# Kernel tuning notes

Hardware: AMD Instinct MI355X
Metric: run time of the kernel (lower is better)

## Reference

```python
import jax, jax.numpy as jnp
import numpy as np

EMBED, IN_DIM, HID, LAYERS, NVIEW = 1024, 256, 256, 3, 6


def _lstm_layer(x_seq, Wih, Whh, bih, bhh):
    # x_seq: [BM, N, D]; torch LSTM gate order i,f,g,o
    BM = x_seq.shape[0]
    h0 = jnp.zeros((BM, HID), x_seq.dtype)
    c0 = jnp.zeros((BM, HID), x_seq.dtype)

    def step(carry, x_t):
        h, c = carry
        gates = x_t @ Wih.T + bih + h @ Whh.T + bhh  # [BM, 4H]
        i, f, g, o = jnp.split(gates, 4, axis=-1)
        c = jax.nn.sigmoid(f) * c + jax.nn.sigmoid(i) * jnp.tanh(g)
        h = jax.nn.sigmoid(o) * jnp.tanh(c)
        return (h, c), h

    _, ys = jax.lax.scan(step, (h0, c0), jnp.swapaxes(x_seq, 0, 1))
    return jnp.swapaxes(ys, 0, 1)  # [BM, N, H]


def setup_inputs() -> dict:
    key = jax.random.key(0)
    ks = jax.random.split(key, 16)
    B, M = 32, 256
    s = lambda fan: 1.0 / np.sqrt(fan)
    inp = {
        "b_x_swin": jax.random.normal(ks[0], (B, M, NVIEW, EMBED), jnp.float32),
        "b_x_conv": jax.random.normal(ks[1], (B, M, NVIEW, EMBED), jnp.float32),
        "Wc": jax.random.uniform(ks[2], (EMBED, EMBED), jnp.float32, -s(EMBED), s(EMBED)),
        "bc": jax.random.uniform(ks[3], (EMBED,), jnp.float32, -s(EMBED), s(EMBED)),
        "Win": jax.random.uniform(ks[4], (IN_DIM, EMBED), jnp.float32, -s(EMBED), s(EMBED)),
        "b_in": jax.random.uniform(ks[5], (IN_DIM,), jnp.float32, -s(EMBED), s(EMBED)),
        "Wih": jax.random.uniform(ks[6], (LAYERS, 4 * HID, IN_DIM), jnp.float32, -s(HID), s(HID)),
        "Whh": jax.random.uniform(ks[7], (LAYERS, 4 * HID, HID), jnp.float32, -s(HID), s(HID)),
        "bih": jax.random.uniform(ks[8], (LAYERS, 4 * HID), jnp.float32, -s(HID), s(HID)),
        "bhh": jax.random.uniform(ks[9], (LAYERS, 4 * HID), jnp.float32, -s(HID), s(HID)),
        "Wv": jax.random.uniform(ks[10], (1, HID), jnp.float32, -s(HID), s(HID)),
        "bv": jax.random.uniform(ks[11], (1,), jnp.float32, -s(HID), s(HID)),
        "Ws": jax.random.uniform(ks[12], (1, NVIEW), jnp.float32, -s(NVIEW), s(NVIEW)),
        "bs": jax.random.uniform(ks[13], (1,), jnp.float32, -s(NVIEW), s(NVIEW)),
    }
    return inp


def reference(b_x_swin, b_x_conv, Wc, bc, Win, b_in, Wih, Whh, bih, bhh, Wv, bv, Ws, bs):
    B, M, N, C = b_x_swin.shape
    # fc_conv + exact GELU + residual (vectorized over all samples; same math as per-sample loop)
    x = b_x_swin + jax.nn.gelu(b_x_conv @ Wc.T + bc, approximate=False)
    x = x @ Win.T + b_in                         # [B, M, N, IN_DIM]
    x = x.reshape(B * M, N, IN_DIM)              # LSTM batch = B*M, seq = N
    for l in range(LAYERS):
        x = _lstm_layer(x, Wih[l], Whh[l], bih[l], bhh[l])
    v = (x @ Wv.T + bv).reshape(B, M, N)         # fc_viewport + flatten(1)
    score = (v @ Ws.T + bs).squeeze(-1)          # fc_score -> [B, M]
    return jnp.mean(score, axis=1)               # torch.mean per sample -> [B]
```

## Files before the change

### kernel.cpp

```cpp
#include <hip/hip_runtime.h>
#include <math.h>
#include <stdint.h>

typedef unsigned short u16;
typedef float f32x4 __attribute__((ext_vector_type(4)));
typedef short bf16x8 __attribute__((ext_vector_type(8)));

#define NVIEW 6

__device__ __forceinline__ u16 f2bf(float f){
  unsigned u = __float_as_uint(f);
  u += 0x7FFFu + ((u >> 16) & 1u);
  return (u16)(u >> 16);
}
__device__ __forceinline__ float bf2f(u16 h){
  return __uint_as_float(((unsigned)h) << 16);
}
__device__ __forceinline__ float fsig(float x){
  x = fminf(fmaxf(x, -30.f), 30.f);
  return 1.0f / (1.0f + __expf(-x));
}
__device__ __forceinline__ float ftanh(float x){
  x = fminf(fmaxf(x, -15.f), 15.f);
  float e = __expf(2.0f * x);
  return (e - 1.0f) / (e + 1.0f);
}
__device__ __forceinline__ float gelu_exact(float v){
  float x  = v * 0.70710678118654752f;
  float ax = fabsf(x);
  float t  = 1.0f / fmaf(0.3275911f, ax, 1.0f);
  float p  = t * fmaf(t, fmaf(t, fmaf(t, fmaf(t, 1.061405429f, -1.453152027f),
                                      1.421413741f), -0.284496736f), 0.254829592f);
  float er = copysignf(1.0f - p * __expf(-ax * ax), x);
  return 0.5f * v * (1.0f + er);
}
__device__ __forceinline__ void gload16(const u16* g, u16* l){
  __builtin_amdgcn_global_load_lds((const __attribute__((address_space(1))) unsigned int*)g,
                                   (__attribute__((address_space(3))) unsigned int*)l,
                                   16, 0, 0);
}

#define DSRI(dst, addr, imm) \
  asm volatile("ds_read_b128 %0, %1 offset:%2" : "=v"(dst) : "v"(addr), "i"(imm))

__global__ void k_cvt(const float* __restrict__ in, u16* __restrict__ out, long n4){
  long i = (long)blockIdx.x * blockDim.x + threadIdx.x;
  long stride = (long)gridDim.x * blockDim.x;
  for (; i < n4; i += stride){
    const float4 v = ((const float4*)in)[i];
    ushort4 o;
    o.x = f2bf(v.x); o.y = f2bf(v.y); o.z = f2bf(v.z); o.w = f2bf(v.w);
    ((ushort4*)out)[i] = o;
  }
}

__global__ void k_build_wl(const float* __restrict__ Wih, const float* __restrict__ Whh,
                           u16* __restrict__ Wl){
  int idx = blockIdx.x * 256 + threadIdx.x;
  int l   = idx >> 19;
  int rem = idx & 524287;
  int ro  = rem >> 9;
  int k   = rem & 511;
  int u = ro >> 2, q = ro & 3;
  int ri = q * 256 + u;
  float v = (k < 256) ? Wih[(l * 1024 + ri) * 256 + k]
                      : Whh[(l * 1024 + ri) * 256 + (k - 256)];
  Wl[idx] = f2bf(v);
}

__global__ void k_build_bias(const float* __restrict__ bih, const float* __restrict__ bhh,
                             float* __restrict__ biasL){
  int idx = blockIdx.x * 256 + threadIdx.x;
  if (idx < 3072){
    int l = idx >> 10; int ro = idx & 1023;
    int u = ro >> 2, q = ro & 3;
    int ri = q * 256 + u;
    biasL[idx] = bih[l * 1024 + ri] + bhh[l * 1024 + ri];
  }
}

template<int EPI>
__global__ __launch_bounds__(256, 2)
void gemm_dr(const u16* __restrict__ A0, long sA0,
             const u16* __restrict__ Bm, long sB,
             int N, int K, int NBn,
             const float* __restrict__ bias,
             const float* __restrict__ resid,
             u16* __restrict__ outb)
{
  __shared__ __align__(16) u16 lA[5 * 4096];
  __shared__ __align__(16) u16 lB[5 * 4096];

  const int tid  = threadIdx.x;
  const int lane = tid & 63;
  const int wid  = tid >> 6;
  const int wm = wid >> 1, wn = wid & 1;
  const int l15 = lane & 15, lk = lane >> 4;

  const int nwg = gridDim.x;
  const int qx  = nwg >> 3;
  const int bb  = blockIdx.x;
  const int swz = (bb & 7) * qx + (bb >> 3);
  const long m0 = (long)(swz / NBn) * 128;
  const int  n0 = (swz % NBn) * 128;
  const int  NT = K >> 5;

  const int rA0 = tid >> 2;
  const int cA  = tid & 3;
  const int slog = (((rA0 & 1) << 2) | cA) ^ ((rA0 >> 1) & 7);
  const int srow = (rA0 & ~1) | (slog >> 2);
  const int scol = (slog & 3) << 3;
  const int ldst = rA0 * 32 + cA * 8;

  auto STAGE = [&](int slot, int t){
    const int kb = t << 5;
    const int so = slot * 4096;
    #pragma unroll
    for (int c = 0; c < 2; ++c){
      const int r  = c * 64 + srow;
      gload16(A0 + (m0 + r) * sA0 + (kb + scol), &lA[so + c * 2048 + ldst]);
    }
    #pragma unroll
    for (int c = 0; c < 2; ++c){
      const int r  = c * 64 + srow;
      gload16(Bm + (long)(n0 + r) * sB + (kb + scol), &lB[so + c * 2048 + ldst]);
    }
  };

  f32x4 acc[4][4];
  #pragma unroll
  for (int i = 0; i < 4; ++i)
    #pragma unroll
    for (int j = 0; j < 4; ++j)
      acc[i][j] = (f32x4){0.f, 0.f, 0.f, 0.f};

  const int spA = (((l15 & 1) << 2) | lk) ^ (l15 >> 1);
  const int rdA = (wm * 32 + (l15 >> 1)) * 64 + spA * 8;
  const int rdB = (wn * 32 + (l15 >> 1)) * 64 + spA * 8;

  auto COMPUTE = [&](int slot){
    const int so = slot * 4096;
    bf16x8 af[4], bq[4];
    #pragma unroll
    for (int mf = 0; mf < 4; ++mf)
      af[mf] = *(const bf16x8*)&lA[so + rdA + mf * 512];
    #pragma unroll
    for (int nf = 0; nf < 4; ++nf)
      bq[nf] = *(const bf16x8*)&lB[so + rdB + nf * 512];
    #pragma unroll
    for (int mf = 0; mf < 4; ++mf)
      #pragma unroll
      for (int nf = 0; nf < 4; ++nf)
        acc[mf][nf] = __builtin_amdgcn_mfma_f32_16x16x32_bf16(af[mf], bq[nf], acc[mf][nf], 0, 0, 0);
  };

  STAGE(0, 0); STAGE(1, 1); STAGE(2, 2); STAGE(3, 3);

  int sr = 0, sw = 4;
  for (int t = 0; t + 4 <= NT; ++t){
    asm volatile("s_waitcnt vmcnt(12)" ::: "memory");
    asm volatile("s_barrier" ::: "memory");
    if (t + 4 < NT){ STAGE(sw, t + 4); }
    COMPUTE(sr);
    sr = (sr == 4) ? 0 : sr + 1;
    sw = (sw == 4) ? 0 : sw + 1;
  }
  asm volatile("s_waitcnt vmcnt(8)" ::: "memory");
  asm volatile("s_barrier" ::: "memory");
  COMPUTE(sr); sr = (sr == 4) ? 0 : sr + 1;
  asm volatile("s_waitcnt vmcnt(4)" ::: "memory");
  asm volatile("s_barrier" ::: "memory");
  COMPUTE(sr); sr = (sr == 4) ? 0 : sr + 1;
  asm volatile("s_waitcnt vmcnt(0)" ::: "memory");
  asm volatile("s_barrier" ::: "memory");
  COMPUTE(sr);

  #pragma unroll
  for (int mf = 0; mf < 4; ++mf){
    #pragma unroll
    for (int nf = 0; nf < 4; ++nf){
      int  n    = n0 + wn * 64 + nf * 16 + l15;
      long mrow = m0 + wm * 64 + mf * 16 + lk * 4;
      float bz = bias[n];
      #pragma unroll
      for (int r = 0; r < 4; ++r){
        float v = acc[mf][nf][r] + bz;
        long off = (mrow + r) * N + n;
        if (EPI == 0) v = gelu_exact(v) + resid[off];
        outb[off] = f2bf(v);
      }
    }
  }
}

__global__ __launch_bounds__(512, 2)
void k_lstm(const u16* __restrict__ X0, const u16* __restrict__ Wl,
            const float* __restrict__ biasL,
            u16* __restrict__ HA, u16* __restrict__ HB)
{
  __shared__ __align__(16) u16 lA[16384];
  __shared__ __align__(16) u16 lB[3 * 16384];

  const int tid  = threadIdx.x;
  const int lane = tid & 63;
  const int wv   = tid >> 6;
  const int wr   = wv >> 2;
  const int wc   = wv & 3;
  const int l15  = lane & 15, lk = lane >> 4;
  const int axk  = l15 & 7;
  const int spB  = (((l15 & 1) << 2) | lk) ^ (l15 >> 1);
  const int a    = lane & 3;
  const int qb   = lane & ~3;
  const long R   = (long)blockIdx.x * 32;
  const int rotk = (blockIdx.x >> 3) & 15;

  const int rB = tid >> 2;
  const int cB = tid & 3;
  const int slogB = (((rB & 1) << 2) | cB) ^ ((rB >> 1) & 7);
  const int srowB = (rB & ~1) | (slogB >> 2);
  const int scolB = (slogB & 3) << 3;
  const int ldstB = rB * 32 + cB * 8;

  auto STB = [&](int P, int l){
    const int hfp  = P & 1;
    const int ktcp = ((P >> 1) + rotk) & 15;
    const int slot = P % 3;
    const u16* src = Wl + (long)l * 524288 + (long)hfp * 262144 + ktcp * 32;
    u16* dst = &lB[slot * 16384];
    #pragma unroll
    for (int ch = 0; ch < 4; ++ch)
      gload16(src + (long)(ch * 128 + srowB) * 512 + scolB, dst + ch * 4096 + ldstB);
  };

  const int xr_ = tid >> 4;
  const int xcb = tid & 15;
  const int xk  = xr_ & 7;

  const unsigned ldsA = (unsigned)(uintptr_t)&lA[0];
  const unsigned ldsB = (unsigned)(uintptr_t)&lB[0];
  const unsigned aRd  = ldsA + (unsigned)((wr * 16 + l15) * 1024);
  const unsigned bRd  = ldsB + (unsigned)((wc * 64 + (l15 >> 1)) * 128 + spB * 16);

  f32x4 acc[2][8];
  float cc[2][8];
  float bv[2][8];

  for (int l = 0; l < 3; ++l){
    const u16* xsrc = (l == 0) ? X0 : ((l == 1) ? HA : HB);
    u16* hdst = (l == 1) ? HB : HA;
    #pragma unroll
    for (int hf = 0; hf < 2; ++hf)
      #pragma unroll
      for (int nt = 0; nt < 8; ++nt){
        bv[hf][nt] = biasL[l * 1024 + hf * 512 + wc * 128 + nt * 16 + l15];
        cc[hf][nt] = 0.f;
      }
    __syncthreads();
    {
      bf16x8 z = (bf16x8){0,0,0,0,0,0,0,0};
      #pragma unroll
      for (int j = 0; j < 2; ++j){
        const int s = xcb * 2 + j;
        *(bf16x8*)&lA[xr_ * 512 + (32 + (s ^ xk)) * 8] = z;
      }
    }
    for (int t = 0; t < 6; ++t){
      bf16x8 xv[2];
      const u16* xp = xsrc + ((R + xr_) * 6 + t) * 256 + xcb * 16;
      xv[0] = *(const bf16x8*)(xp);
      xv[1] = *(const bf16x8*)(xp + 8);
      asm volatile("s_waitcnt vmcnt(0)" ::: "memory");
      #pragma unroll
      for (int hf = 0; hf < 2; ++hf)
        #pragma unroll
        for (int nt = 0; nt < 8; ++nt)
          acc[hf][nt] = (f32x4){0.f, 0.f, 0.f, 0.f};
      #pragma unroll
      for (int j = 0; j < 2; ++j){
        const int s = xcb * 2 + j;
        *(bf16x8*)&lA[xr_ * 512 + (s ^ xk) * 8] = xv[j];
      }
      STB(0, l); STB(1, l);
      asm volatile("s_waitcnt lgkmcnt(0)" ::: "memory");
      __builtin_amdgcn_s_barrier();

      for (int j = 0; j < 16; ++j){
        const int ktc = (j + rotk) & 15;
        const unsigned aAddr = aRd + (unsigned)((((ktc * 4 + lk) ^ axk)) << 4);
        #pragma unroll
        for (int hh = 0; hh < 2; ++hh){
          const int P = 2 * j + hh;
          if (P == 31) { asm volatile("s_waitcnt vmcnt(0)" ::: "memory"); }
          else         { asm volatile("s_waitcnt vmcnt(4)" ::: "memory"); }
          __builtin_amdgcn_s_barrier();
          if (P + 2 < 32) STB(P + 2, l);
          bf16x8 af, bq[8];
          DSRI(af, aAddr, 0);
          const unsigned bAddr = bRd + (unsigned)((P % 3) * 32768);
          DSRI(bq[0], bAddr, 0);
          DSRI(bq[1], bAddr, 1024);
          DSRI(bq[2], bAddr, 2048);
          DSRI(bq[3], bAddr, 3072);
          DSRI(bq[4], bAddr, 4096);
          DSRI(bq[5], bAddr, 5120);
          DSRI(bq[6], bAddr, 6144);
          DSRI(bq[7], bAddr, 7168);
          asm volatile("s_waitcnt lgkmcnt(0)" ::: "memory");
          __builtin_amdgcn_sched_barrier(0);
          __builtin_amdgcn_s_setprio(1);
          #pragma unroll
          for (int nt = 0; nt < 8; ++nt)
            acc[hh][nt] = __builtin_amdgcn_mfma_f32_16x16x32_bf16(af, bq[nt], acc[hh][nt], 0, 0, 0);
          __builtin_amdgcn_s_setprio(0);
        }
      }
      __builtin_amdgcn_s_barrier();

      #pragma unroll
      for (int hf = 0; hf < 2; ++hf)
        #pragma unroll
        for (int nt = 0; nt < 8; ++nt){
          const float bz = bv[hf][nt];
          float v0 = acc[hf][nt][0] + bz;
          float v1 = acc[hf][nt][1] + bz;
          float v2 = acc[hf][nt][2] + bz;
          float v3 = acc[hf][nt][3] + bz;
          float s0 = (a == 0) ? v0 : (a == 1) ? v1 : (a == 2) ? v2 : v3;
          float s1 = (a == 0) ? v1 : (a == 1) ? v2 : (a == 2) ? v3 : v0;
          float s2 = (a == 0) ? v2 : (a == 1) ? v3 : (a == 2) ? v0 : v1;
          float s3 = (a == 0) ? v3 : (a == 1) ? v0 : (a == 2) ? v1 : v2;
          float r0 = s0;
          float r1 = __shfl(s1, qb + ((a + 3) & 3));
          float r2 = __shfl(s2, qb + ((a + 2) & 3));
          float r3 = __shfl(s3, qb + ((a + 1) & 3));
          float wi = (a == 0) ? r0 : (a == 1) ? r1 : (a == 2) ? r2 : r3;
          float wf = (a == 1) ? r0 : (a == 2) ? r1 : (a == 3) ? r2 : r3;
          float wg = (a == 2) ? r0 : (a == 3) ? r1 : (a == 0) ? r2 : r3;
          float wo = (a == 3) ? r0 : (a == 0) ? r1 : (a == 1) ? r2 : r3;
          const int rloc = wr * 16 + lk * 4 + a;
          const int u    = hf * 128 + wc * 32 + nt * 4 + (l15 >> 2);
          float co = cc[hf][nt];
          float ii = fsig(wi), ff = fsig(wf), gg = ftanh(wg), oo = fsig(wo);
          float cn = ff * co + ii * gg;
          float hn = oo * ftanh(cn);
          cc[hf][nt] = cn;
          lA[rloc * 512 + (32 + ((u >> 3) ^ (rloc & 7))) * 8 + (u & 7)] = f2bf(hn);
        }
      asm volatile("s_waitcnt lgkmcnt(0)" ::: "memory");
      __builtin_amdgcn_s_barrier();
      #pragma unroll
      for (int j2 = 0; j2 < 2; ++j2){
        const int s = xcb * 2 + j2;
        bf16x8 hv = *(const bf16x8*)&lA[xr_ * 512 + (32 + (s ^ xk)) * 8];
        *(bf16x8*)(hdst + ((R + xr_) * 6 + t) * 256 + xcb * 16 + j2 * 8) = hv;
      }
    }
  }
}

__global__ void k_score(const u16* __restrict__ X3, const float* __restrict__ Wv,
                        const float* __restrict__ bv, const float* __restrict__ Ws,
                        const float* __restrict__ bs, float* __restrict__ score){
  int lane = threadIdx.x & 63;
  int bm = blockIdx.x * 4 + (threadIdx.x >> 6);
  const u16* row = X3 + (long)bm * (NVIEW * 256);
  float4 wv = *(const float4*)(Wv + lane * 4);
  float p = 0.f;
  #pragma unroll
  for (int n = 0; n < NVIEW; ++n){
    ushort4 xv = *(const ushort4*)(row + n * 256 + lane * 4);
    float d = bf2f(xv.x) * wv.x + bf2f(xv.y) * wv.y + bf2f(xv.z) * wv.z + bf2f(xv.w) * wv.w;
    p += Ws[n] * d;
  }
  #pragma unroll
  for (int off = 32; off; off >>= 1) p += __shfl_xor(p, off);
  if (lane == 0){
    float sw = Ws[0] + Ws[1] + Ws[2] + Ws[3] + Ws[4] + Ws[5];
    score[bm] = p + bv[0] * sw + bs[0];
  }
}

__global__ void k_mean(const float* __restrict__ score, float* __restrict__ out){
  __shared__ float red[256];
  int b = blockIdx.x, tid = threadIdx.x;
  red[tid] = score[b * 256 + tid];
  __syncthreads();
  for (int s = 128; s > 0; s >>= 1){
    if (tid < s) red[tid] += red[tid + s];
    __syncthreads();
  }
  if (tid == 0) out[b] = red[0] * (1.0f / 256.0f);
}

extern "C" void kernel_launch(void* const* d_in, const int* in_sizes, int n_in,
                              void* d_out, int out_size, void* d_ws, size_t ws_size,
                              hipStream_t stream){
  const float* swin = (const float*)d_in[0];
  const float* conv = (const float*)d_in[1];
  const float* Wc   = (const float*)d_in[2];
  const float* bc   = (const float*)d_in[3];
  const float* Win  = (const float*)d_in[4];
  const float* b_in = (const float*)d_in[5];
  const float* Wih  = (const float*)d_in[6];
  const float* Whh  = (const float*)d_in[7];
  const float* bih  = (const float*)d_in[8];
  const float* bhh  = (const float*)d_in[9];
  const float* Wv   = (const float*)d_in[10];
  const float* bv   = (const float*)d_in[11];
  const float* Ws   = (const float*)d_in[12];
  const float* bs   = (const float*)d_in[13];
  float* out = (float*)d_out;

  char* w = (char*)d_ws;
  u16*  convb = (u16*)(w);
  u16*  X0    = (u16*)(w);
  u16*  XA    = (u16*)(w + 25165824);
  u16*  XB    = (u16*)(w + 50331648);
  u16*  Y     = (u16*)(w + 100663296);
  u16*  Wcb   = (u16*)(w + 201326592);
  u16*  Winb  = (u16*)(w + 203423744);
  u16*  Wl    = (u16*)(w + 203948032);
  float* biasL= (float*)(w + 207093760);
  float* scoreb = (float*)(w + 207106560);

  k_cvt<<<4096, 256, 0, stream>>>(conv, convb, 49152L * 1024 / 4);
  k_cvt<<<512, 256, 0, stream>>>(Wc, Wcb, 1048576 / 4);
  k_cvt<<<128, 256, 0, stream>>>(Win, Winb, 262144 / 4);
  k_build_wl<<<6144, 256, 0, stream>>>(Wih, Whh, Wl);
  k_build_bias<<<12, 256, 0, stream>>>(bih, bhh, biasL);

  gemm_dr<0><<<3072, 256, 0, stream>>>(
      convb, 1024L, Wcb, 1024L, 1024, 1024, 8, bc, swin, Y);

  gemm_dr<1><<<768, 256, 0, stream>>>(
      Y, 1024L, Winb, 1024L, 256, 1024, 2, b_in, (const float*)nullptr, X0);

  k_lstm<<<256, 512, 0, stream>>>(X0, Wl, biasL, XA, XB);

  k_score<<<2048, 256, 0, stream>>>(XA, Wv, bv, Ws, bs, scoreb);
  k_mean<<<32, 256, 0, stream>>>(scoreb, out);
}
```

Measured before the change: 739.7 us.

## Load LSTM weight fragments directly from global into registers, dropping LDS staging

The LSTM recurrence kernel no longer stages gate weights into a triple-buffered shared-memory ring with global_load_lds. Each wave now loads its own weight fragments straight from global memory into a double-buffered register set. Waves are re-partitioned so that each one covers all 32 rows and 128 gate columns, instead of a 2x4 grid of 16-row slices. This removes most per-k-step barriers and the LDS round trip for weights. In exchange it raises register pressure (two 8-fragment buffers plus a larger accumulator tile) under launch_bounds(512,2), which risks spills, and it leaves global-load latency covered by only one prefetch stage.

After: 932.3 us. 1.26x slower.

```diff
diff --git a/kernel.cpp b/kernel.cpp
--- a/kernel.cpp
+++ b/kernel.cpp
@@ -39,9 +39,6 @@
                                    (__attribute__((address_space(3))) unsigned int*)l,
                                    16, 0, 0);
 }
-
-#define DSRI(dst, addr, imm) \
-  asm volatile("ds_read_b128 %0, %1 offset:%2" : "=v"(dst) : "v"(addr), "i"(imm))
 
 __global__ void k_cvt(const float* __restrict__ in, u16* __restrict__ out, long n4){
   long i = (long)blockIdx.x * blockDim.x + threadIdx.x;
@@ -199,62 +196,35 @@
             u16* __restrict__ HA, u16* __restrict__ HB)
 {
   __shared__ __align__(16) u16 lA[16384];
-  __shared__ __align__(16) u16 lB[3 * 16384];
 
   const int tid  = threadIdx.x;
   const int lane = tid & 63;
   const int wv   = tid >> 6;
-  const int wr   = wv >> 2;
-  const int wc   = wv & 3;
   const int l15  = lane & 15, lk = lane >> 4;
   const int axk  = l15 & 7;
-  const int spB  = (((l15 & 1) << 2) | lk) ^ (l15 >> 1);
   const int a    = lane & 3;
   const int qb   = lane & ~3;
   const long R   = (long)blockIdx.x * 32;
   const int rotk = (blockIdx.x >> 3) & 15;
-
-  const int rB = tid >> 2;
-  const int cB = tid & 3;
-  const int slogB = (((rB & 1) << 2) | cB) ^ ((rB >> 1) & 7);
-  const int srowB = (rB & ~1) | (slogB >> 2);
-  const int scolB = (slogB & 3) << 3;
-  const int ldstB = rB * 32 + cB * 8;
-
-  auto STB = [&](int P, int l){
-    const int hfp  = P & 1;
-    const int ktcp = ((P >> 1) + rotk) & 15;
-    const int slot = P % 3;
-    const u16* src = Wl + (long)l * 524288 + (long)hfp * 262144 + ktcp * 32;
-    u16* dst = &lB[slot * 16384];
-    #pragma unroll
-    for (int ch = 0; ch < 4; ++ch)
-      gload16(src + (long)(ch * 128 + srowB) * 512 + scolB, dst + ch * 4096 + ldstB);
-  };
+  const int gb   = wv * 128;
 
   const int xr_ = tid >> 4;
   const int xcb = tid & 15;
   const int xk  = xr_ & 7;
 
-  const unsigned ldsA = (unsigned)(uintptr_t)&lA[0];
-  const unsigned ldsB = (unsigned)(uintptr_t)&lB[0];
-  const unsigned aRd  = ldsA + (unsigned)((wr * 16 + l15) * 1024);
-  const unsigned bRd  = ldsB + (unsigned)((wc * 64 + (l15 >> 1)) * 128 + spB * 16);
-
   f32x4 acc[2][8];
   float cc[2][8];
-  float bv[2][8];
+  float bv[8];
 
   for (int l = 0; l < 3; ++l){
     const u16* xsrc = (l == 0) ? X0 : ((l == 1) ? HA : HB);
     u16* hdst = (l == 1) ? HB : HA;
-    #pragma unroll
-    for (int hf = 0; hf < 2; ++hf)
-      #pragma unroll
-      for (int nt = 0; nt < 8; ++nt){
-        bv[hf][nt] = biasL[l * 1024 + hf * 512 + wc * 128 + nt * 16 + l15];
-        cc[hf][nt] = 0.f;
-      }
+    const u16* wbase = Wl + (long)l * 524288 + (long)(gb + l15) * 512 + lk * 8;
+    #pragma unroll
+    for (int nt = 0; nt < 8; ++nt){
+      bv[nt] = biasL[l * 1024 + gb + nt * 16 + l15];
+      cc[0][nt] = 0.f; cc[1][nt] = 0.f;
+    }
     __syncthreads();
     {
       bf16x8 z = (bf16x8){0,0,0,0,0,0,0,0};
@@ -265,66 +235,72 @@
       }
     }
     for (int t = 0; t < 6; ++t){
-      bf16x8 xv[2];
+      bf16x8 xv0, xv1;
       const u16* xp = xsrc + ((R + xr_) * 6 + t) * 256 + xcb * 16;
-      xv[0] = *(const bf16x8*)(xp);
-      xv[1] = *(const bf16x8*)(xp + 8);
-      asm volatile("s_waitcnt vmcnt(0)" ::: "memory");
+      xv0 = *(const bf16x8*)(xp);
+      xv1 = *(const bf16x8*)(xp + 8);
       #pragma unroll
-      for (int hf = 0; hf < 2; ++hf)
+      for (int mt = 0; mt < 2; ++mt)
         #pragma unroll
         for (int nt = 0; nt < 8; ++nt)
-          acc[hf][nt] = (f32x4){0.f, 0.f, 0.f, 0.f};
-      #pragma unroll
-      for (int j = 0; j < 2; ++j){
-        const int s = xcb * 2 + j;
-        *(bf16x8*)&lA[xr_ * 512 + (s ^ xk) * 8] = xv[j];
+          acc[mt][nt] = (f32x4){0.f, 0.f, 0.f, 0.f};
+      {
+        const int s0 = xcb * 2;
+        *(bf16x8*)&lA[xr_ * 512 + (s0 ^ xk) * 8] = xv0;
+        *(bf16x8*)&lA[xr_ * 512 + ((s0 + 1) ^ xk) * 8] = xv1;
       }
-      STB(0, l); STB(1, l);
-      asm volatile("s_waitcnt lgkmcnt(0)" ::: "memory");
-      __builtin_amdgcn_s_barrier();
-
-      for (int j = 0; j < 16; ++j){
+      __syncthreads();
+
+      bf16x8 bqA[8], bqB[8];
+      auto LOADB = [&](bf16x8* bq, int j){
         const int ktc = (j + rotk) & 15;
-        const unsigned aAddr = aRd + (unsigned)((((ktc * 4 + lk) ^ axk)) << 4);
+        const u16* bp = wbase + ktc * 32;
         #pragma unroll
-        for (int hh = 0; hh < 2; ++hh){
-          const int P = 2 * j + hh;
-          if (P == 31) { asm volatile("s_waitcnt vmcnt(0)" ::: "memory"); }
-          else         { asm volatile("s_waitcnt vmcnt(4)" ::: "memory"); }
-          __builtin_amdgcn_s_barrier();
-          if (P + 2 < 32) STB(P + 2, l);
-          bf16x8 af, bq[8];
-          DSRI(af, aAddr, 0);
-          const unsigned bAddr = bRd + (unsigned)((P % 3) * 32768);
-          DSRI(bq[0], bAddr, 0);
-          DSRI(bq[1], bAddr, 1024);
-          DSRI(bq[2], bAddr, 2048);
-          DSRI(bq[3], bAddr, 3072);
-          DSRI(bq[4], bAddr, 4096);
-          DSRI(bq[5], bAddr, 5120);
-          DSRI(bq[6], bAddr, 6144);
-          DSRI(bq[7], bAddr, 7168);
-          asm volatile("s_waitcnt lgkmcnt(0)" ::: "memory");
-          __builtin_amdgcn_sched_barrier(0);
+        for (int nt = 0; nt < 8; ++nt)
+          bq[nt] = *(const bf16x8*)(bp + (long)nt * 8192);
+      };
+      auto READA = [&](bf16x8* af, int j){
+        const int ktc = (j + rotk) & 15;
+        #pragma unroll
+        for (int mt = 0; mt < 2; ++mt)
+          af[mt] = *(const bf16x8*)&lA[(mt * 16 + l15) * 512 + ((ktc * 4 + lk) ^ axk) * 8];
+      };
+      LOADB(bqA, 0);
+      for (int jj = 0; jj < 8; ++jj){
+        LOADB(bqB, 2 * jj + 1);
+        {
+          bf16x8 af[2]; READA(af, 2 * jj);
           __builtin_amdgcn_s_setprio(1);
           #pragma unroll
-          for (int nt = 0; nt < 8; ++nt)
-            acc[hh][nt] = __builtin_amdgcn_mfma_f32_16x16x32_bf16(af, bq[nt], acc[hh][nt], 0, 0, 0);
+          for (int mt = 0; mt < 2; ++mt)
+            #pragma unroll
+            for (int nt = 0; nt < 8; ++nt)
+              acc[mt][nt] = __builtin_amdgcn_mfma_f32_16x16x32_bf16(af[mt], bqA[nt], acc[mt][nt], 0, 0, 0);
+          __builtin_amdgcn_s_setprio(0);
+        }
+        if (jj < 7) LOADB(bqA, 2 * jj + 2);
+        {
+          bf16x8 af[2]; READA(af, 2 * jj + 1);
+          __builtin_amdgcn_s_setprio(1);
+          #pragma unroll
+          for (int mt = 0; mt < 2; ++mt)
+            #pragma unroll
+            for (int nt = 0; nt < 8; ++nt)
+              acc[mt][nt] = __builtin_amdgcn_mfma_f32_16x16x32_bf16(af[mt], bqB[nt], acc[mt][nt], 0, 0, 0);
           __builtin_amdgcn_s_setprio(0);
         }
       }
-      __builtin_amdgcn_s_barrier();
+      __syncthreads();
 
       #pragma unroll
-      for (int hf = 0; hf < 2; ++hf)
+      for (int mt = 0; mt < 2; ++mt)
         #pragma unroll
         for (int nt = 0; nt < 8; ++nt){
-          const float bz = bv[hf][nt];
-          float v0 = acc[hf][nt][0] + bz;
-          float v1 = acc[hf][nt][1] + bz;
-          float v2 = acc[hf][nt][2] + bz;
-          float v3 = acc[hf][nt][3] + bz;
+          const float bz = bv[nt];
+          float v0 = acc[mt][nt][0] + bz;
+          float v1 = acc[mt][nt][1] + bz;
+          float v2 = acc[mt][nt][2] + bz;
+          float v3 = acc[mt][nt][3] + bz;
           float s0 = (a == 0) ? v0 : (a == 1) ? v1 : (a == 2) ? v2 : v3;
           float s1 = (a == 0) ? v1 : (a == 1) ? v2 : (a == 2) ? v3 : v0;
           float s2 = (a == 0) ? v2 : (a == 1) ? v3 : (a == 2) ? v0 : v1;
@@ -337,22 +313,22 @@
           float wf = (a == 1) ? r0 : (a == 2) ? r1 : (a == 3) ? r2 : r3;
           float wg = (a == 2) ? r0 : (a == 3) ? r1 : (a == 0) ? r2 : r3;
           float wo = (a == 3) ? r0 : (a == 0) ? r1 : (a == 1) ? r2 : r3;
-          const int rloc = wr * 16 + lk * 4 + a;
-          const int u    = hf * 128 + wc * 32 + nt * 4 + (l15 >> 2);
-          float co = cc[hf][nt];
+          const int rloc = mt * 16 + lk * 4 + a;
+          const int u    = wv * 32 + nt * 4 + (l15 >> 2);
+          float co = cc[mt][nt];
           float ii = fsig(wi), ff = fsig(wf), gg = ftanh(wg), oo = fsig(wo);
           float cn = ff * co + ii * gg;
           float hn = oo * ftanh(cn);
-          cc[hf][nt] = cn;
+          cc[mt][nt] = cn;
           lA[rloc * 512 + (32 + ((u >> 3) ^ (rloc & 7))) * 8 + (u & 7)] = f2bf(hn);
         }
-      asm volatile("s_waitcnt lgkmcnt(0)" ::: "memory");
-      __builtin_amdgcn_s_barrier();
-      #pragma unroll
-      for (int j2 = 0; j2 < 2; ++j2){
-        const int s = xcb * 2 + j2;
-        bf16x8 hv = *(const bf16x8*)&lA[xr_ * 512 + (32 + (s ^ xk)) * 8];
-        *(bf16x8*)(hdst + ((R + xr_) * 6 + t) * 256 + xcb * 16 + j2 * 8) = hv;
+      __syncthreads();
+      {
+        const int s0 = xcb * 2;
+        bf16x8 h0 = *(const bf16x8*)&lA[xr_ * 512 + (32 + (s0 ^ xk)) * 8];
+        bf16x8 h1 = *(const bf16x8*)&lA[xr_ * 512 + (32 + ((s0 + 1) ^ xk)) * 8];
+        *(bf16x8*)(hdst + ((R + xr_) * 6 + t) * 256 + xcb * 16) = h0;
+        *(bf16x8*)(hdst + ((R + xr_) * 6 + t) * 256 + xcb * 16 + 8) = h1;
       }
     }
   }
```
